# Kernel tuning notes

Measured on AMD Instinct MI355X. Metric: run time of the kernel, lower is better.

The kernel has to match this reference:

```python
import jax, jax.numpy as jnp
import numpy as np
from jax import lax

DILATIONS = (1, 2, 4, 8)
PADDINGS = (4, 8, 16, 32)  # 2p = 8d -> 'same' length for kernel 9


def setup_inputs() -> dict:
    key = jax.random.key(0)
    ks = jax.random.split(key, 8)
    B, Ci, H, W = 16, 128, 64, 64
    inp = {}
    for i in range(4):
        inp[f"x{i+1}"] = jax.random.normal(ks[i], (B, Ci, H, W), dtype=jnp.float32)
    inp["conv_w"] = jax.random.normal(ks[4], (4, 1, 1, 9), dtype=jnp.float32) * 0.3
    inp["conv_b"] = jax.random.normal(ks[5], (4,), dtype=jnp.float32) * 0.1
    inp["lin_w"] = jax.random.normal(ks[6], (1, 4), dtype=jnp.float32) * 0.5
    inp["lin_b"] = jax.random.normal(ks[7], (1,), dtype=jnp.float32) * 0.1
    return inp


def reference(x1, x2, x3, x4, conv_w, conv_b, lin_w, lin_b):
    # map1: [B, C, H, W] with C = sum of channels
    map1 = jnp.concatenate([x1, x2, x3, x4], axis=1)
    # global average pool -> [B, 1, C] treated as 1D sequence over channels
    gp = jnp.mean(map1, axis=(2, 3))            # [B, C]
    seq = gp[:, None, :]                        # [B, 1, C]
    branch_outs = []
    for i, (d, p) in enumerate(zip(DILATIONS, PADDINGS)):
        o = lax.conv_general_dilated(
            seq, conv_w[i],                     # [B,1,C] x [1,1,9]
            window_strides=(1,),
            padding=[(p, p)],
            rhs_dilation=(d,),
            dimension_numbers=("NCH", "OIH", "NCH"),
        ) + conv_b[i]
        branch_outs.append(o)                   # each [B,1,C]
    cat = jnp.concatenate(branch_outs, axis=1)  # [B,4,C]
    feat = jax.nn.relu(jnp.transpose(cat, (0, 2, 1)))  # [B,C,4]
    lin = jnp.einsum("bcf,of->bco", feat, lin_w) + lin_b  # [B,C,1]
    gate = jax.nn.sigmoid(lin)[..., None]       # [B,C,1,1]
    return gate * map1
```

## Files before the change

kernel.cpp:

```cpp
#include <hip/hip_runtime.h>
#include <math.h>

#define PLANES   8192
#define PLANE_SZ 4096
#define CHANS    512
#define NBLK     2048
#define PPB      2
#define FLAG_SET 0xC0FFEE42u

typedef float f32x4 __attribute__((ext_vector_type(4)));

__global__ __launch_bounds__(256, 4) void fused_kernel(
    const float* __restrict__ x1, const float* __restrict__ x2,
    const float* __restrict__ x3, const float* __restrict__ x4,
    const float* __restrict__ conv_w, const float* __restrict__ conv_b,
    const float* __restrict__ lin_w,  const float* __restrict__ lin_b,
    float* __restrict__ gp, unsigned* __restrict__ flags,
    float* __restrict__ out)
{
    const int tid  = threadIdx.x;
    const int blk  = blockIdx.x;
    const int bat1 = blk >> 8;
    const int bat2 = bat1 + 8;
    const int lb   = blk & 255;
    const int c1   = lb * PPB;
    const int pA1  = bat1 * CHANS + c1;
    const int pA2  = bat2 * CHANS + c1;
    const int xi   = c1 >> 7;
    const float* srcb = (xi == 0) ? x1 : (xi == 1) ? x2 : (xi == 2) ? x3 : x4;
    const f32x4* p4a = (const f32x4*)(srcb + (size_t)(bat1 * 128 + (c1 & 127)) * PLANE_SZ);
    const f32x4* p4b = (const f32x4*)(srcb + (size_t)(bat2 * 128 + (c1 & 127)) * PLANE_SZ);

    __shared__ float gwin[PPB + 64];
    __shared__ float wsum1[PPB][4], wsum2[PPB][4];
    __shared__ float gates[PPB];

    const int lane = tid & 63, wv = tid >> 6;
    const int lo = (lb - 16 < 0) ? 0 : lb - 16;
    const int hi = (lb + 16 > 255) ? 255 : lb + 16;
    const int base = blk & ~255;

    f32x4 v1[PPB][4];
    #pragma unroll
    for (int p = 0; p < PPB; ++p)
        #pragma unroll
        for (int j = 0; j < 4; ++j)
            v1[p][j] = __builtin_nontemporal_load(&p4a[p * 1024 + j * 256 + tid]);
    {
        float s[PPB];
        #pragma unroll
        for (int p = 0; p < PPB; ++p) {
            f32x4 t = (v1[p][0] + v1[p][1]) + (v1[p][2] + v1[p][3]);
            s[p] = (t.x + t.y) + (t.z + t.w);
        }
        #pragma unroll
        for (int off = 32; off > 0; off >>= 1)
            #pragma unroll
            for (int p = 0; p < PPB; ++p)
                s[p] += __shfl_down(s[p], off, 64);
        if (lane == 0)
            #pragma unroll
            for (int p = 0; p < PPB; ++p)
                wsum1[p][wv] = s[p];
    }
    __syncthreads();
    if (tid < PPB) {
        float m = ((wsum1[tid][0] + wsum1[tid][1]) +
                   (wsum1[tid][2] + wsum1[tid][3])) * (1.0f / PLANE_SZ);
        __hip_atomic_store(&gp[pA1 + tid], m, __ATOMIC_RELAXED, __HIP_MEMORY_SCOPE_AGENT);
    }
    #pragma unroll
    for (int p = 0; p < PPB; ++p)
        #pragma unroll
        for (int j = 0; j < 4; ++j)
            asm volatile("" : "+v"(v1[p][j]));
    if (tid == 0) {
        asm volatile("s_waitcnt vmcnt(0)" ::: "memory");
        __hip_atomic_store(&flags[blk * 16], FLAG_SET, __ATOMIC_RELAXED, __HIP_MEMORY_SCOPE_AGENT);
    }

    f32x4 v2[PPB][4];
    #pragma unroll
    for (int p = 0; p < PPB; ++p)
        #pragma unroll
        for (int j = 0; j < 4; ++j)
            v2[p][j] = __builtin_nontemporal_load(&p4b[p * 1024 + j * 256 + tid]);
    {
        float s[PPB];
        #pragma unroll
        for (int p = 0; p < PPB; ++p) {
            f32x4 t = (v2[p][0] + v2[p][1]) + (v2[p][2] + v2[p][3]);
            s[p] = (t.x + t.y) + (t.z + t.w);
        }
        #pragma unroll
        for (int off = 32; off > 0; off >>= 1)
            #pragma unroll
            for (int p = 0; p < PPB; ++p)
                s[p] += __shfl_down(s[p], off, 64);
        if (lane == 0)
            #pragma unroll
            for (int p = 0; p < PPB; ++p)
                wsum2[p][wv] = s[p];
    }
    __syncthreads();
    if (tid < PPB) {
        float m = ((wsum2[tid][0] + wsum2[tid][1]) +
                   (wsum2[tid][2] + wsum2[tid][3])) * (1.0f / PLANE_SZ);
        __hip_atomic_store(&gp[pA2 + tid], m, __ATOMIC_RELAXED, __HIP_MEMORY_SCOPE_AGENT);
    }
    #pragma unroll
    for (int p = 0; p < PPB; ++p)
        #pragma unroll
        for (int j = 0; j < 4; ++j)
            asm volatile("" : "+v"(v2[p][j]));
    if (tid == 0) {
        asm volatile("s_waitcnt vmcnt(0)" ::: "memory");
        __hip_atomic_store(&flags[blk * 16 + 4], FLAG_SET, __ATOMIC_RELAXED, __HIP_MEMORY_SCOPE_AGENT);
    }
    __syncthreads();

    if (tid <= hi - lo) {
        const unsigned* f = &flags[(base + lo + tid) * 16];
        while (__hip_atomic_load(f, __ATOMIC_RELAXED, __HIP_MEMORY_SCOPE_AGENT) != FLAG_SET)
            __builtin_amdgcn_s_sleep(8);
    }
    __syncthreads();
    asm volatile("" ::: "memory");
    if (tid < PPB + 64) {
        int idx = c1 - 32 + tid;
        gwin[tid] = (idx >= 0 && idx < CHANS)
            ? __hip_atomic_load(&gp[bat1 * CHANS + idx], __ATOMIC_RELAXED, __HIP_MEMORY_SCOPE_AGENT)
            : 0.f;
    }
    __syncthreads();
    if (tid < PPB) {
        float lin = lin_b[0];
        #pragma unroll
        for (int i = 0; i < 4; ++i) {
            const int d = 1 << i;
            float acc = conv_b[i];
            #pragma unroll
            for (int k = 0; k < 9; ++k)
                acc += conv_w[i * 9 + k] * gwin[32 + tid + d * (k - 4)];
            lin += lin_w[i] * fmaxf(acc, 0.f);
        }
        gates[tid] = 1.0f / (1.0f + expf(-lin));
    }
    __syncthreads();
    {
        f32x4* o4 = (f32x4*)(out + (size_t)pA1 * PLANE_SZ);
        #pragma unroll
        for (int p = 0; p < PPB; ++p) {
            const float gv = gates[p];
            #pragma unroll
            for (int j = 0; j < 4; ++j) {
                f32x4 t = v1[p][j] * gv;
                __builtin_nontemporal_store(t, &o4[p * 1024 + j * 256 + tid]);
            }
        }
    }
    __syncthreads();

    if (tid <= hi - lo) {
        const unsigned* f = &flags[(base + lo + tid) * 16 + 4];
        while (__hip_atomic_load(f, __ATOMIC_RELAXED, __HIP_MEMORY_SCOPE_AGENT) != FLAG_SET)
            __builtin_amdgcn_s_sleep(8);
    }
    __syncthreads();
    asm volatile("" ::: "memory");
    if (tid < PPB + 64) {
        int idx = c1 - 32 + tid;
        gwin[tid] = (idx >= 0 && idx < CHANS)
            ? __hip_atomic_load(&gp[bat2 * CHANS + idx], __ATOMIC_RELAXED, __HIP_MEMORY_SCOPE_AGENT)
            : 0.f;
    }
    __syncthreads();
    if (tid < PPB) {
        float lin = lin_b[0];
        #pragma unroll
        for (int i = 0; i < 4; ++i) {
            const int d = 1 << i;
            float acc = conv_b[i];
            #pragma unroll
            for (int k = 0; k < 9; ++k)
                acc += conv_w[i * 9 + k] * gwin[32 + tid + d * (k - 4)];
            lin += lin_w[i] * fmaxf(acc, 0.f);
        }
        gates[tid] = 1.0f / (1.0f + expf(-lin));
    }
    __syncthreads();
    {
        f32x4* o4 = (f32x4*)(out + (size_t)pA2 * PLANE_SZ);
        #pragma unroll
        for (int p = 0; p < PPB; ++p) {
            const float gv = gates[p];
            #pragma unroll
            for (int j = 0; j < 4; ++j) {
                f32x4 t = v2[p][j] * gv;
                __builtin_nontemporal_store(t, &o4[p * 1024 + j * 256 + tid]);
            }
        }
    }
}

extern "C" void kernel_launch(void* const* d_in, const int* in_sizes, int n_in,
                              void* d_out, int out_size, void* d_ws, size_t ws_size,
                              hipStream_t stream) {
    const float* x1     = (const float*)d_in[0];
    const float* x2     = (const float*)d_in[1];
    const float* x3     = (const float*)d_in[2];
    const float* x4     = (const float*)d_in[3];
    const float* conv_w = (const float*)d_in[4];
    const float* conv_b = (const float*)d_in[5];
    const float* lin_w  = (const float*)d_in[6];
    const float* lin_b  = (const float*)d_in[7];
    float* out = (float*)d_out;

    float*    gp    = (float*)d_ws;
    unsigned* flags = (unsigned*)((char*)d_ws + PLANES * sizeof(float));

    fused_kernel<<<NBLK, 256, 0, stream>>>(x1, x2, x3, x4,
                                           conv_w, conv_b, lin_w, lin_b,
                                           gp, flags, out);
}
```

Measured before the change: 51.04 us.

## Load both batch planes together and merge the two flag/gate phases

Each block now issues the loads for both of its batch planes at once, reduces them together and publishes both channel means behind one flag. It then waits on one set of neighbor flags, computes both gate sets in separate thread groups, and writes both outputs in one pass. This removes the staggered two-phase schedule with its second spin-wait and extra barriers, and keeps more memory requests in flight per block. In exchange, every block holds both planes in registers before any store, and no global-pool store or output write overlaps with a later load anymore.

```diff
diff --git a/kernel.cpp b/kernel.cpp
--- a/kernel.cpp
+++ b/kernel.cpp
@@ -31,91 +31,65 @@
     const f32x4* p4a = (const f32x4*)(srcb + (size_t)(bat1 * 128 + (c1 & 127)) * PLANE_SZ);
     const f32x4* p4b = (const f32x4*)(srcb + (size_t)(bat2 * 128 + (c1 & 127)) * PLANE_SZ);
 
-    __shared__ float gwin[PPB + 64];
+    __shared__ float gwin1[PPB + 64], gwin2[PPB + 64];
     __shared__ float wsum1[PPB][4], wsum2[PPB][4];
-    __shared__ float gates[PPB];
+    __shared__ float gates1[PPB], gates2[PPB];
 
     const int lane = tid & 63, wv = tid >> 6;
     const int lo = (lb - 16 < 0) ? 0 : lb - 16;
     const int hi = (lb + 16 > 255) ? 255 : lb + 16;
     const int base = blk & ~255;
 
-    f32x4 v1[PPB][4];
+    f32x4 v1[PPB][4], v2[PPB][4];
     #pragma unroll
     for (int p = 0; p < PPB; ++p)
         #pragma unroll
-        for (int j = 0; j < 4; ++j)
+        for (int j = 0; j < 4; ++j) {
             v1[p][j] = __builtin_nontemporal_load(&p4a[p * 1024 + j * 256 + tid]);
-    {
-        float s[PPB];
+            v2[p][j] = __builtin_nontemporal_load(&p4b[p * 1024 + j * 256 + tid]);
+        }
+
+    float s1[PPB], s2[PPB];
+    #pragma unroll
+    for (int p = 0; p < PPB; ++p) {
+        f32x4 t1 = (v1[p][0] + v1[p][1]) + (v1[p][2] + v1[p][3]);
+        f32x4 t2 = (v2[p][0] + v2[p][1]) + (v2[p][2] + v2[p][3]);
+        s1[p] = (t1.x + t1.y) + (t1.z + t1.w);
+        s2[p] = (t2.x + t2.y) + (t2.z + t2.w);
+    }
+    #pragma unroll
+    for (int off = 32; off > 0; off >>= 1)
         #pragma unroll
         for (int p = 0; p < PPB; ++p) {
-            f32x4 t = (v1[p][0] + v1[p][1]) + (v1[p][2] + v1[p][3]);
-            s[p] = (t.x + t.y) + (t.z + t.w);
+            s1[p] += __shfl_down(s1[p], off, 64);
+            s2[p] += __shfl_down(s2[p], off, 64);
         }
+    if (lane == 0)
         #pragma unroll
-        for (int off = 32; off > 0; off >>= 1)
-            #pragma unroll
-            for (int p = 0; p < PPB; ++p)
-                s[p] += __shfl_down(s[p], off, 64);
-        if (lane == 0)
-            #pragma unroll
-            for (int p = 0; p < PPB; ++p)
-                wsum1[p][wv] = s[p];
-    }
+        for (int p = 0; p < PPB; ++p) {
+            wsum1[p][wv] = s1[p];
+            wsum2[p][wv] = s2[p];
+        }
     __syncthreads();
+
     if (tid < PPB) {
-        float m = ((wsum1[tid][0] + wsum1[tid][1]) +
-                   (wsum1[tid][2] + wsum1[tid][3])) * (1.0f / PLANE_SZ);
-        __hip_atomic_store(&gp[pA1 + tid], m, __ATOMIC_RELAXED, __HIP_MEMORY_SCOPE_AGENT);
+        float m1 = ((wsum1[tid][0] + wsum1[tid][1]) +
+                    (wsum1[tid][2] + wsum1[tid][3])) * (1.0f / PLANE_SZ);
+        float m2 = ((wsum2[tid][0] + wsum2[tid][1]) +
+                    (wsum2[tid][2] + wsum2[tid][3])) * (1.0f / PLANE_SZ);
+        __hip_atomic_store(&gp[pA1 + tid], m1, __ATOMIC_RELAXED, __HIP_MEMORY_SCOPE_AGENT);
+        __hip_atomic_store(&gp[pA2 + tid], m2, __ATOMIC_RELAXED, __HIP_MEMORY_SCOPE_AGENT);
     }
     #pragma unroll
     for (int p = 0; p < PPB; ++p)
         #pragma unroll
-        for (int j = 0; j < 4; ++j)
+        for (int j = 0; j < 4; ++j) {
             asm volatile("" : "+v"(v1[p][j]));
+            asm volatile("" : "+v"(v2[p][j]));
+        }
     if (tid == 0) {
         asm volatile("s_waitcnt vmcnt(0)" ::: "memory");
         __hip_atomic_store(&flags[blk * 16], FLAG_SET, __ATOMIC_RELAXED, __HIP_MEMORY_SCOPE_AGENT);
-    }
-
-    f32x4 v2[PPB][4];
-    #pragma unroll
-    for (int p = 0; p < PPB; ++p)
-        #pragma unroll
-        for (int j = 0; j < 4; ++j)
-            v2[p][j] = __builtin_nontemporal_load(&p4b[p * 1024 + j * 256 + tid]);
-    {
-        float s[PPB];
-        #pragma unroll
-        for (int p = 0; p < PPB; ++p) {
-            f32x4 t = (v2[p][0] + v2[p][1]) + (v2[p][2] + v2[p][3]);
-            s[p] = (t.x + t.y) + (t.z + t.w);
-        }
-        #pragma unroll
-        for (int off = 32; off > 0; off >>= 1)
-            #pragma unroll
-            for (int p = 0; p < PPB; ++p)
-                s[p] += __shfl_down(s[p], off, 64);
-        if (lane == 0)
-            #pragma unroll
-            for (int p = 0; p < PPB; ++p)
-                wsum2[p][wv] = s[p];
-    }
-    __syncthreads();
-    if (tid < PPB) {
-        float m = ((wsum2[tid][0] + wsum2[tid][1]) +
-                   (wsum2[tid][2] + wsum2[tid][3])) * (1.0f / PLANE_SZ);
-        __hip_atomic_store(&gp[pA2 + tid], m, __ATOMIC_RELAXED, __HIP_MEMORY_SCOPE_AGENT);
-    }
-    #pragma unroll
-    for (int p = 0; p < PPB; ++p)
-        #pragma unroll
-        for (int j = 0; j < 4; ++j)
-            asm volatile("" : "+v"(v2[p][j]));
-    if (tid == 0) {
-        asm volatile("s_waitcnt vmcnt(0)" ::: "memory");
-        __hip_atomic_store(&flags[blk * 16 + 4], FLAG_SET, __ATOMIC_RELAXED, __HIP_MEMORY_SCOPE_AGENT);
     }
     __syncthreads();
 
@@ -126,13 +100,20 @@
     }
     __syncthreads();
     asm volatile("" ::: "memory");
+
     if (tid < PPB + 64) {
         int idx = c1 - 32 + tid;
-        gwin[tid] = (idx >= 0 && idx < CHANS)
+        gwin1[tid] = (idx >= 0 && idx < CHANS)
             ? __hip_atomic_load(&gp[bat1 * CHANS + idx], __ATOMIC_RELAXED, __HIP_MEMORY_SCOPE_AGENT)
+            : 0.f;
+    } else if (tid >= 128 && tid < 128 + PPB + 64) {
+        int idx = c1 - 32 + (tid - 128);
+        gwin2[tid - 128] = (idx >= 0 && idx < CHANS)
+            ? __hip_atomic_load(&gp[bat2 * CHANS + idx], __ATOMIC_RELAXED, __HIP_MEMORY_SCOPE_AGENT)
             : 0.f;
     }
     __syncthreads();
+
     if (tid < PPB) {
         float lin = lin_b[0];
         #pragma unroll
@@ -141,41 +122,12 @@
             float acc = conv_b[i];
             #pragma unroll
             for (int k = 0; k < 9; ++k)
-                acc += conv_w[i * 9 + k] * gwin[32 + tid + d * (k - 4)];
+                acc += conv_w[i * 9 + k] * gwin1[32 + tid + d * (k - 4)];
             lin += lin_w[i] * fmaxf(acc, 0.f);
         }
-        gates[tid] = 1.0f / (1.0f + expf(-lin));
-    }
-    __syncthreads();
-    {
-        f32x4* o4 = (f32x4*)(out + (size_t)pA1 * PLANE_SZ);
-        #pragma unroll
-        for (int p = 0; p < PPB; ++p) {
-            const float gv = gates[p];
-            #pragma unroll
-            for (int j = 0; j < 4; ++j) {
-                f32x4 t = v1[p][j] * gv;
-                __builtin_nontemporal_store(t, &o4[p * 1024 + j * 256 + tid]);
-            }
-        }
-    }
-    __syncthreads();
-
-    if (tid <= hi - lo) {
-        const unsigned* f = &flags[(base + lo + tid) * 16 + 4];
-        while (__hip_atomic_load(f, __ATOMIC_RELAXED, __HIP_MEMORY_SCOPE_AGENT) != FLAG_SET)
-            __builtin_amdgcn_s_sleep(8);
-    }
-    __syncthreads();
-    asm volatile("" ::: "memory");
-    if (tid < PPB + 64) {
-        int idx = c1 - 32 + tid;
-        gwin[tid] = (idx >= 0 && idx < CHANS)
-            ? __hip_atomic_load(&gp[bat2 * CHANS + idx], __ATOMIC_RELAXED, __HIP_MEMORY_SCOPE_AGENT)
-            : 0.f;
-    }
-    __syncthreads();
-    if (tid < PPB) {
+        gates1[tid] = 1.0f / (1.0f + expf(-lin));
+    } else if (tid >= 128 && tid < 128 + PPB) {
+        const int t = tid - 128;
         float lin = lin_b[0];
         #pragma unroll
         for (int i = 0; i < 4; ++i) {
@@ -183,21 +135,25 @@
             float acc = conv_b[i];
             #pragma unroll
             for (int k = 0; k < 9; ++k)
-                acc += conv_w[i * 9 + k] * gwin[32 + tid + d * (k - 4)];
+                acc += conv_w[i * 9 + k] * gwin2[32 + t + d * (k - 4)];
             lin += lin_w[i] * fmaxf(acc, 0.f);
         }
-        gates[tid] = 1.0f / (1.0f + expf(-lin));
+        gates2[t] = 1.0f / (1.0f + expf(-lin));
     }
     __syncthreads();
+
     {
-        f32x4* o4 = (f32x4*)(out + (size_t)pA2 * PLANE_SZ);
+        f32x4* o4a = (f32x4*)(out + (size_t)pA1 * PLANE_SZ);
+        f32x4* o4b = (f32x4*)(out + (size_t)pA2 * PLANE_SZ);
         #pragma unroll
         for (int p = 0; p < PPB; ++p) {
-            const float gv = gates[p];
+            const float g1 = gates1[p], g2 = gates2[p];
             #pragma unroll
             for (int j = 0; j < 4; ++j) {
-                f32x4 t = v2[p][j] * gv;
-                __builtin_nontemporal_store(t, &o4[p * 1024 + j * 256 + tid]);
+                f32x4 t1 = v1[p][j] * g1;
+                f32x4 t2 = v2[p][j] * g2;
+                __builtin_nontemporal_store(t1, &o4a[p * 1024 + j * 256 + tid]);
+                __builtin_nontemporal_store(t2, &o4b[p * 1024 + j * 256 + tid]);
             }
         }
     }
```

Result: no change. 52.06 us (+2.0%).
